# Performance work log

Measured on AMD Instinct MI355X. Metric: run time of the kernel, lower is better.

## Reference

```python
import jax, jax.numpy as jnp
import numpy as np

B, S, D, H, O = 4, 128, 768, 768, 2

def setup_inputs() -> dict:
    key = jax.random.key(0)
    ks = jax.random.split(key, 6)
    scale = 1.0 / np.sqrt(2 * D)
    return {
        "a": jax.random.normal(ks[0], (B, S, D), jnp.float32),
        "b": jax.random.normal(ks[1], (B, S, D), jnp.float32),
        "W1": jax.random.normal(ks[2], (2 * D, H), jnp.float32) * scale,
        "b1": jax.random.normal(ks[3], (H,), jnp.float32) * 0.01,
        "W2": jax.random.normal(ks[4], (H, O), jnp.float32) * (1.0 / np.sqrt(H)),
        "b2": jax.random.normal(ks[5], (O,), jnp.float32) * 0.01,
    }

def reference(a, b, W1, b1, W2, b2):
    # Pairwise concat [a_i ; b_j] followed by Linear(2D->H) is algebraically
    # identical to projecting a and b separately and broadcast-adding
    # (biaffine-style rewrite; same math as cat+matmul, less HBM traffic).
    d = a.shape[-1]
    ha = jnp.einsum('bsd,dh->bsh', a, W1[:d])        # (B, Sa, H)
    hb = jnp.einsum('btd,dh->bth', b, W1[d:])        # (B, Sb, H)
    h = jax.nn.relu(ha[:, :, None, :] + hb[:, None, :, :] + b1)  # (B, Sa, Sb, H)
    scores = jnp.einsum('bsth,ho->bsto', h, W2) + b2  # (B, Sa, Sb, O)
    return scores
```

## Files before the change

kernel.cpp:

```cpp
#include <hip/hip_runtime.h>
#include <hip/hip_fp16.h>


typedef __attribute__((ext_vector_type(2))) _Float16 half2t;
typedef __attribute__((ext_vector_type(8))) _Float16 half8t;
typedef __attribute__((ext_vector_type(4))) float floatx4;
typedef unsigned int uint;

__device__ __forceinline__ half2t pkrtz(float x, float y) {
    __fp16 r __attribute__((ext_vector_type(2))) = __builtin_amdgcn_cvt_pkrtz(x, y);
    half2t o; __builtin_memcpy(&o, &r, 4); return o;
}

__global__ __launch_bounds__(256) void gemm_kernel(
    const float* __restrict__ a, const float* __restrict__ bmat,
    const float* __restrict__ W1, const float* __restrict__ b1,
    ushort* __restrict__ Hf)
{
    const int which = blockIdx.z;
    const int n0 = blockIdx.x * 64;
    const int m0 = blockIdx.y * 64;
    const int t  = threadIdx.x;

    __shared__ ushort As[64][40];
    __shared__ ushort Bs[64][40];

    const int srow = t >> 2;
    const int skc  = (t & 3) * 8;
    const float* __restrict__ Asrc = which ? bmat : a;
    const float* __restrict__ aptr = Asrc + (size_t)(m0 + srow) * 768 + skc;

    const int ncolS = t & 63;
    const int kg0   = (t >> 6) * 8;
    const float* __restrict__ bptr = W1 + (size_t)(which * 768 + kg0) * 768 + n0 + ncolS;

    float4 af0 = *(const float4*)(aptr);
    float4 af1 = *(const float4*)(aptr + 4);
    float breg[8];
#pragma unroll
    for (int j = 0; j < 8; j++) breg[j] = bptr[(size_t)j * 768];

    const int lane = t & 63;
    const int w    = t >> 6;
    const int lr   = lane & 15;
    const int lq   = lane >> 4;

    floatx4 acc0 = {0,0,0,0}, acc1 = {0,0,0,0}, acc2 = {0,0,0,0}, acc3 = {0,0,0,0};

    for (int kt = 0; kt < 768; kt += 32) {
        __syncthreads();
        half2t ap[4];
        ap[0] = pkrtz(af0.x, af0.y);
        ap[1] = pkrtz(af0.z, af0.w);
        ap[2] = pkrtz(af1.x, af1.y);
        ap[3] = pkrtz(af1.z, af1.w);
        __builtin_memcpy(&As[srow][skc], ap, 16);
        half2t bp[4];
        bp[0] = pkrtz(breg[0], breg[1]);
        bp[1] = pkrtz(breg[2], breg[3]);
        bp[2] = pkrtz(breg[4], breg[5]);
        bp[3] = pkrtz(breg[6], breg[7]);
        __builtin_memcpy(&Bs[ncolS][kg0], bp, 16);
        __syncthreads();

        if (kt + 32 < 768) {
            af0 = *(const float4*)(aptr + kt + 32);
            af1 = *(const float4*)(aptr + kt + 36);
#pragma unroll
            for (int j = 0; j < 8; j++) breg[j] = bptr[(size_t)(kt + 32 + j) * 768];
        }

        half8t bfr, a0, a1, a2, a3;
        __builtin_memcpy(&bfr, &Bs[w * 16 + lr][lq * 8], 16);
        __builtin_memcpy(&a0,  &As[     lr][lq * 8], 16);
        __builtin_memcpy(&a1,  &As[16 + lr][lq * 8], 16);
        __builtin_memcpy(&a2,  &As[32 + lr][lq * 8], 16);
        __builtin_memcpy(&a3,  &As[48 + lr][lq * 8], 16);
        acc0 = __builtin_amdgcn_mfma_f32_16x16x32_f16(a0, bfr, acc0, 0, 0, 0);
        acc1 = __builtin_amdgcn_mfma_f32_16x16x32_f16(a1, bfr, acc1, 0, 0, 0);
        acc2 = __builtin_amdgcn_mfma_f32_16x16x32_f16(a2, bfr, acc2, 0, 0, 0);
        acc3 = __builtin_amdgcn_mfma_f32_16x16x32_f16(a3, bfr, acc3, 0, 0, 0);
    }

    const int ncol = n0 + w * 16 + lr;
    const float bias = which ? 0.f : b1[ncol];
    ushort* __restrict__ dst = Hf + (size_t)which * 393216 + ncol;
    const int rbase = m0 + lq * 4;
#pragma unroll
    for (int r = 0; r < 4; r++) {
        _Float16 v0 = (_Float16)(acc0[r] + bias);
        _Float16 v1 = (_Float16)(acc1[r] + bias);
        _Float16 v2 = (_Float16)(acc2[r] + bias);
        _Float16 v3 = (_Float16)(acc3[r] + bias);
        ushort u0, u1, u2, u3;
        __builtin_memcpy(&u0, &v0, 2); __builtin_memcpy(&u1, &v1, 2);
        __builtin_memcpy(&u2, &v2, 2); __builtin_memcpy(&u3, &v3, 2);
        dst[(size_t)(rbase +      r) * 768] = u0;
        dst[(size_t)(rbase + 16 + r) * 768] = u1;
        dst[(size_t)(rbase + 32 + r) * 768] = u2;
        dst[(size_t)(rbase + 48 + r) * 768] = u3;
    }
}

__global__ __launch_bounds__(256) void pair_kernel(
    const ushort* __restrict__ Hf, const float* __restrict__ W2,
    const float* __restrict__ b2, float* __restrict__ out)
{
    const int bb = blockIdx.z;
    const int s0 = blockIdx.y * 16;
    const int t0 = blockIdx.x * 16;
    const int tid = threadIdx.x;

    __shared__ ushort hAs[16][776];
    __shared__ ushort hBs[16][776];
    __shared__ uint w2s[768];

    const ushort* __restrict__ Asrc = Hf +          (size_t)(bb * 128 + s0) * 768;
    const ushort* __restrict__ Bsrc = Hf + 393216 + (size_t)(bb * 128 + t0) * 768;

#pragma unroll
    for (int i = 0; i < 6; i++) {
        const int c   = tid + i * 256;
        const int row = c / 96;
        const int col = (c % 96) * 8;
        *(uint4*)&hAs[row][col] = *(const uint4*)(Asrc + (size_t)row * 768 + col);
        *(uint4*)&hBs[row][col] = *(const uint4*)(Bsrc + (size_t)row * 768 + col);
    }
#pragma unroll
    for (int j = tid; j < 768; j += 256) {
        const int o  = (j >= 384) ? 1 : 0;
        const int h2 = j - o * 384;
        half2t p = pkrtz(W2[4 * h2 + o], W2[4 * h2 + 2 + o]);
        uint u; __builtin_memcpy(&u, &p, 4);
        w2s[j] = u;
    }
    __syncthreads();

    const int sl = tid >> 4;
    const int tl = tid & 15;
    const ushort* __restrict__ arow = &hAs[sl][0];
    const ushort* __restrict__ brow = &hBs[tl][0];

    float acc0 = 0.f, acc1 = 0.f;
    const half2t zero = {(_Float16)0.f, (_Float16)0.f};

#pragma unroll 8
    for (int h8 = 0; h8 < 768; h8 += 8) {
        half2t pa[4], pb[4], w0[4], w1[4];
        __builtin_memcpy(pa, arow + h8, 16);
        __builtin_memcpy(pb, brow + h8, 16);
        __builtin_memcpy(w0, &w2s[h8 / 2], 16);
        __builtin_memcpy(w1, &w2s[384 + h8 / 2], 16);
#pragma unroll
        for (int j = 0; j < 4; j++) {
            half2t s = pa[j] + pb[j];
            s = __builtin_elementwise_max(s, zero);
            acc0 = __builtin_amdgcn_fdot2(s, w0[j], acc0, false);
            acc1 = __builtin_amdgcn_fdot2(s, w1[j], acc1, false);
        }
    }

    const int sg = bb * 128 + s0 + sl;
    const int tg = t0 + tl;
    float2 r = make_float2(acc0 + b2[0], acc1 + b2[1]);
    *(float2*)&out[((size_t)sg * 128 + tg) * 2] = r;
}

extern "C" void kernel_launch(void* const* d_in, const int* in_sizes, int n_in,
                              void* d_out, int out_size, void* d_ws, size_t ws_size,
                              hipStream_t stream) {
    const float* a  = (const float*)d_in[0];
    const float* b  = (const float*)d_in[1];
    const float* W1 = (const float*)d_in[2];
    const float* b1 = (const float*)d_in[3];
    const float* W2 = (const float*)d_in[4];
    const float* b2 = (const float*)d_in[5];
    float* out = (float*)d_out;

    ushort* Hf = (ushort*)d_ws;

    gemm_kernel<<<dim3(12, 8, 2), 256, 0, stream>>>(a, b, W1, b1, Hf);
    pair_kernel<<<dim3(8, 8, 4), 256, 0, stream>>>(Hf, W2, b2, out);
}
```

Before: 89.06 us.

## Double-buffer GEMM shared tiles and widen K step to 64

The projection GEMM now processes 64 K-elements per iteration using two ping-pong shared-memory buffers, so only one barrier is needed per step instead of two. Each thread prefetches twice as many A and W1 values into registers for the next tile. This is meant to cut barrier and loop overhead and expose more memory-level parallelism, at the cost of higher register and shared-memory use per block.

Result: no change. 88.99 us (-0.1%).

```diff
diff --git a/kernel.cpp b/kernel.cpp
--- a/kernel.cpp
+++ b/kernel.cpp
@@ -22,23 +22,17 @@
     const int m0 = blockIdx.y * 64;
     const int t  = threadIdx.x;
 
-    __shared__ ushort As[64][40];
-    __shared__ ushort Bs[64][40];
+    __shared__ ushort As[2][64][72];
+    __shared__ ushort Bs[2][64][72];
 
-    const int srow = t >> 2;
-    const int skc  = (t & 3) * 8;
+    const int arow = t >> 2;
+    const int akc  = (t & 3) * 16;
     const float* __restrict__ Asrc = which ? bmat : a;
-    const float* __restrict__ aptr = Asrc + (size_t)(m0 + srow) * 768 + skc;
+    const float* __restrict__ aptr = Asrc + (size_t)(m0 + arow) * 768 + akc;
 
-    const int ncolS = t & 63;
-    const int kg0   = (t >> 6) * 8;
-    const float* __restrict__ bptr = W1 + (size_t)(which * 768 + kg0) * 768 + n0 + ncolS;
-
-    float4 af0 = *(const float4*)(aptr);
-    float4 af1 = *(const float4*)(aptr + 4);
-    float breg[8];
-#pragma unroll
-    for (int j = 0; j < 8; j++) breg[j] = bptr[(size_t)j * 768];
+    const int ncol = t & 63;
+    const int kg   = (t >> 6) * 16;
+    const float* __restrict__ bptr = W1 + (size_t)(which * 768 + kg) * 768 + n0 + ncol;
 
     const int lane = t & 63;
     const int w    = t >> 6;
@@ -47,44 +41,59 @@
 
     floatx4 acc0 = {0,0,0,0}, acc1 = {0,0,0,0}, acc2 = {0,0,0,0}, acc3 = {0,0,0,0};
 
-    for (int kt = 0; kt < 768; kt += 32) {
-        __syncthreads();
-        half2t ap[4];
-        ap[0] = pkrtz(af0.x, af0.y);
-        ap[1] = pkrtz(af0.z, af0.w);
-        ap[2] = pkrtz(af1.x, af1.y);
-        ap[3] = pkrtz(af1.z, af1.w);
-        __builtin_memcpy(&As[srow][skc], ap, 16);
-        half2t bp[4];
-        bp[0] = pkrtz(breg[0], breg[1]);
-        bp[1] = pkrtz(breg[2], breg[3]);
-        bp[2] = pkrtz(breg[4], breg[5]);
-        bp[3] = pkrtz(breg[6], breg[7]);
-        __builtin_memcpy(&Bs[ncolS][kg0], bp, 16);
+    float4 a4[4];
+    float  br[16];
+#pragma unroll
+    for (int i = 0; i < 4; i++) a4[i] = *(const float4*)(aptr + 4 * i);
+#pragma unroll
+    for (int j = 0; j < 16; j++) br[j] = bptr[(size_t)j * 768];
+
+    int p = 0;
+    for (int kt = 0; kt < 768; kt += 64, p ^= 1) {
+        half2t ap[8];
+#pragma unroll
+        for (int i = 0; i < 4; i++) {
+            ap[2 * i    ] = pkrtz(a4[i].x, a4[i].y);
+            ap[2 * i + 1] = pkrtz(a4[i].z, a4[i].w);
+        }
+        __builtin_memcpy(&As[p][arow][akc],     &ap[0], 16);
+        __builtin_memcpy(&As[p][arow][akc + 8], &ap[4], 16);
+        half2t bp[8];
+#pragma unroll
+        for (int j = 0; j < 8; j++) bp[j] = pkrtz(br[2 * j], br[2 * j + 1]);
+        __builtin_memcpy(&Bs[p][ncol][kg],     &bp[0], 16);
+        __builtin_memcpy(&Bs[p][ncol][kg + 8], &bp[4], 16);
+
         __syncthreads();
 
-        if (kt + 32 < 768) {
-            af0 = *(const float4*)(aptr + kt + 32);
-            af1 = *(const float4*)(aptr + kt + 36);
+        if (kt + 64 < 768) {
 #pragma unroll
-            for (int j = 0; j < 8; j++) breg[j] = bptr[(size_t)(kt + 32 + j) * 768];
+            for (int i = 0; i < 4; i++)
+                a4[i] = *(const float4*)(aptr + kt + 64 + 4 * i);
+#pragma unroll
+            for (int j = 0; j < 16; j++)
+                br[j] = bptr[(size_t)(kt + 64 + j) * 768];
         }
 
-        half8t bfr, a0, a1, a2, a3;
-        __builtin_memcpy(&bfr, &Bs[w * 16 + lr][lq * 8], 16);
-        __builtin_memcpy(&a0,  &As[     lr][lq * 8], 16);
-        __builtin_memcpy(&a1,  &As[16 + lr][lq * 8], 16);
-        __builtin_memcpy(&a2,  &As[32 + lr][lq * 8], 16);
-        __builtin_memcpy(&a3,  &As[48 + lr][lq * 8], 16);
-        acc0 = __builtin_amdgcn_mfma_f32_16x16x32_f16(a0, bfr, acc0, 0, 0, 0);
-        acc1 = __builtin_amdgcn_mfma_f32_16x16x32_f16(a1, bfr, acc1, 0, 0, 0);
-        acc2 = __builtin_amdgcn_mfma_f32_16x16x32_f16(a2, bfr, acc2, 0, 0, 0);
-        acc3 = __builtin_amdgcn_mfma_f32_16x16x32_f16(a3, bfr, acc3, 0, 0, 0);
+#pragma unroll
+        for (int h = 0; h < 2; h++) {
+            const int kb = h * 32 + lq * 8;
+            half8t bfr, f0, f1, f2, f3;
+            __builtin_memcpy(&bfr, &Bs[p][w * 16 + lr][kb], 16);
+            __builtin_memcpy(&f0,  &As[p][     lr][kb], 16);
+            __builtin_memcpy(&f1,  &As[p][16 + lr][kb], 16);
+            __builtin_memcpy(&f2,  &As[p][32 + lr][kb], 16);
+            __builtin_memcpy(&f3,  &As[p][48 + lr][kb], 16);
+            acc0 = __builtin_amdgcn_mfma_f32_16x16x32_f16(f0, bfr, acc0, 0, 0, 0);
+            acc1 = __builtin_amdgcn_mfma_f32_16x16x32_f16(f1, bfr, acc1, 0, 0, 0);
+            acc2 = __builtin_amdgcn_mfma_f32_16x16x32_f16(f2, bfr, acc2, 0, 0, 0);
+            acc3 = __builtin_amdgcn_mfma_f32_16x16x32_f16(f3, bfr, acc3, 0, 0, 0);
+        }
     }
 
-    const int ncol = n0 + w * 16 + lr;
-    const float bias = which ? 0.f : b1[ncol];
-    ushort* __restrict__ dst = Hf + (size_t)which * 393216 + ncol;
+    const int ncolO = n0 + w * 16 + lr;
+    const float bias = which ? 0.f : b1[ncolO];
+    ushort* __restrict__ dst = Hf + (size_t)which * 393216 + ncolO;
     const int rbase = m0 + lq * 4;
 #pragma unroll
     for (int r = 0; r < 4; r++) {
```
